# Performance work log

Hardware: AMD Instinct MI355X
Metric: run time of the kernel (lower is better)

Reference implementation:

```python
import jax, jax.numpy as jnp
import numpy as np

REG = 0.1  # config['reg']


def _poly_filter(s, gammas):
    # Horner evaluation of sum_k gammas[k] * s**k (monomial basis, depth K=len-1).
    out = jnp.full_like(s, gammas[-1])
    for k in range(gammas.shape[0] - 2, -1, -1):
        out = out * s + gammas[k]
    return out


def setup_inputs() -> dict:
    key = jax.random.key(0)
    k1, k2, k3, k4, k5 = jax.random.split(key, 5)
    B, H, N, R = 4, 8, 4096, 64
    U = jax.random.normal(k1, (B, H, N, R), dtype=jnp.float32)
    Sigma = jax.random.normal(k2, (B, H, 1, R), dtype=jnp.float32)
    svd_V = jax.random.normal(k3, (B, H, N, R), dtype=jnp.float32)
    V = jax.random.normal(k4, (B, H, N, R), dtype=jnp.float32)
    mask = jnp.ones((B, N), dtype=jnp.float32)
    # learnable polynomial coefficients; gamma_0 fixed to 1 (fixI=True)
    gammas = jnp.concatenate([jnp.ones((1,), jnp.float32),
                              0.1 * jax.random.normal(k5, (4,), dtype=jnp.float32)])
    return {"U": U, "Sigma": Sigma, "svd_V": svd_V, "V": V, "mask": mask, "gammas": gammas}


def reference(U, Sigma, svd_V, V, mask, gammas):
    # Q: softmax over rank dim r
    Q = jax.nn.softmax(U, axis=-1)                                      # [B,H,N,r]
    # K: masked softmax over sequence dim N
    Kmat = jax.nn.softmax(svd_V - 1e9 * (1.0 - mask[:, None, :, None]), axis=-2)
    S = jax.nn.sigmoid(Sigma)                                           # [B,H,1,r]
    graph_filter = _poly_filter(S, gammas)                              # [B,H,1,r]
    # linear-attention ordering: (Q*filt) @ (K^T @ V), never forms NxN
    KtV = jnp.einsum('bhnr,bhnd->bhrd', Kmat, V)                        # [B,H,r,d]
    X = jnp.einsum('bhnr,bhrd->bhnd', Q * graph_filter, KtV)            # [B,H,N,d]
    r = Q.shape[-1]
    eye = jnp.eye(r, dtype=Q.dtype)
    symQ = jnp.einsum('bhnr,bhns->bhrs', Q, Q) - eye
    ortho_loss = REG * jnp.mean(jnp.abs(symQ), axis=(1, 2, 3))
    symK = jnp.einsum('bhnr,bhns->bhrs', Kmat, Kmat) - eye
    ortho_loss = ortho_loss + REG * jnp.mean(jnp.abs(symK), axis=(1, 2, 3))
    return X, ortho_loss
```

## Files before the change

### kernel.cpp

```cpp
#include <hip/hip_runtime.h>
#include <math.h>

#define NB 4
#define NH 8
#define BHN 32
#define SN 4096
#define RR 64
#define REGC 0.1f

#define MCH 16
#define MROWS 256
#define XCH 32
#define XROWS 128

typedef short s16x8 __attribute__((ext_vector_type(8)));
typedef float f32x4 __attribute__((ext_vector_type(4)));

__device__ __forceinline__ float wave_sum(float v) {
    #pragma unroll
    for (int off = 32; off; off >>= 1) v += __shfl_xor(v, off, 64);
    return v;
}
__device__ __forceinline__ float wave_sum64(float v) {
    v += __int_as_float(__builtin_amdgcn_update_dpp(0, __float_as_int(v), 0x121, 0xf, 0xf, true));
    v += __int_as_float(__builtin_amdgcn_update_dpp(0, __float_as_int(v), 0x122, 0xf, 0xf, true));
    v += __int_as_float(__builtin_amdgcn_update_dpp(0, __float_as_int(v), 0x124, 0xf, 0xf, true));
    v += __int_as_float(__builtin_amdgcn_update_dpp(0, __float_as_int(v), 0x128, 0xf, 0xf, true));
    v += __shfl_xor(v, 16, 64);
    v += __shfl_xor(v, 32, 64);
    return v;
}
__device__ __forceinline__ float octet_sum(float v) {
    v += __int_as_float(__builtin_amdgcn_update_dpp(0, __float_as_int(v), 0xB1, 0xf, 0xf, true));
    v += __int_as_float(__builtin_amdgcn_update_dpp(0, __float_as_int(v), 0x4E, 0xf, 0xf, true));
    v += __shfl_xor(v, 4, 64);
    return v;
}
__device__ __forceinline__ float fastrcp(float x) {
    float r; asm("v_rcp_f32 %0, %1" : "=v"(r) : "v"(x)); return r;
}
__device__ __forceinline__ unsigned short f2bf(float x) {
    unsigned int u = __float_as_uint(x);
    u += 0x7FFFu + ((u >> 16) & 1u);
    return (unsigned short)(u >> 16);
}
__device__ __forceinline__ float bf2f(unsigned short h) {
    return __uint_as_float(((unsigned int)h) << 16);
}
__device__ __forceinline__ unsigned int pkbf(float lo, float hi) {
    unsigned int r;
    asm("v_cvt_pk_bf16_f32 %0, %1, %2" : "=v"(r) : "v"(lo), "v"(hi));
    return r;
}
__device__ __forceinline__ void barrier_nodrain() {
    asm volatile("s_waitcnt lgkmcnt(0)" ::: "memory");
    __builtin_amdgcn_s_barrier();
}
__device__ __forceinline__ s16x8 ldfrag(const unsigned int* p) {
    uint4 r = *(const uint4*)p;
    return __builtin_bit_cast(s16x8, r);
}
__device__ __forceinline__ int swz(int row, int blk) {
    return (row << 5) + (((blk ^ (row & 7))) << 2);
}
__device__ __forceinline__ uint4 pack8(const float* x) {
    return make_uint4(pkbf(x[0], x[1]), pkbf(x[2], x[3]),
                      pkbf(x[4], x[5]), pkbf(x[6], x[7]));
}

#define PH 0
#define VH 2048
#define QH 4096
__launch_bounds__(512, 4)
__global__ void k_main(const float* __restrict__ U, const float* __restrict__ sv,
                       const float* __restrict__ V, const float* __restrict__ mask,
                       float* __restrict__ ktv_part, float* __restrict__ symk_part,
                       float* __restrict__ symq_part, float* __restrict__ colsum_part) {
    __shared__ __align__(16) unsigned int sm[12288];
    const int chunk = blockIdx.x, bh = blockIdx.y, b = bh >> 3;
    const int t = threadIdx.x, l = t & 63, w = t >> 6;
    const int r15 = l & 15, quad = l >> 4;
    const int ni = w & 3, mi0 = (w >> 2) << 1;
    const size_t rowbase = (size_t)bh * SN * RR;
    const int row0 = chunk * MROWS;

    float csum = 0.0f;
    f32x4 aKV[2], aSK[2], aSQ[2];
    #pragma unroll
    for (int j = 0; j < 2; j++) {
        aKV[j] = (f32x4){0.f, 0.f, 0.f, 0.f};
        aSK[j] = (f32x4){0.f, 0.f, 0.f, 0.f};
        aSQ[j] = (f32x4){0.f, 0.f, 0.f, 0.f};
    }

    float bu[2][8], bx[2][8], bv[2][8], bm[2][8];
    #pragma unroll
    for (int i = 0; i < 8; i++) {
        const size_t off = rowbase + (size_t)(row0 + 8 * w + i) * RR + l;
        bu[0][i] = __builtin_nontemporal_load(&U[off]);
        bx[0][i] = __builtin_nontemporal_load(&sv[off]);
        bv[0][i] = __builtin_nontemporal_load(&V[off]);
        bm[0][i] = mask[b * SN + row0 + 8 * w + i];
    }

    #pragma unroll
    for (int s = 0; s < 4; s++) {
        const int cur = s & 1, nxt = cur ^ 1;
        const int nb = row0 + s * 64;
        const int bufb = cur * 6144;
        if (s < 3) {
            #pragma unroll
            for (int i = 0; i < 8; i++) {
                const size_t off = rowbase + (size_t)(nb + 64 + 8 * w + i) * RR + l;
                bu[nxt][i] = __builtin_nontemporal_load(&U[off]);
                bx[nxt][i] = __builtin_nontemporal_load(&sv[off]);
                bv[nxt][i] = __builtin_nontemporal_load(&V[off]);
                bm[nxt][i] = mask[b * SN + nb + 64 + 8 * w + i];
            }
        }
        float q[8], p[8];
        #pragma unroll
        for (int i = 0; i < 8; i++) {
            const float eu = __expf(bu[cur][i]);
            q[i] = eu * fastrcp(wave_sum64(eu));
        }
        #pragma unroll
        for (int i = 0; i < 8; i++) {
            p[i] = __expf(bx[cur][i] - 1e9f * (1.0f - bm[cur][i]));
            csum += p[i];
        }
        const uint4 ph = pack8(p);
        const uint4 vh = pack8(bv[cur]);
        const uint4 qh = pack8(q);
        const int wbase = bufb + (l << 5) + ((w ^ (l & 7)) << 2);
        *(uint4*)(sm + PH + wbase) = ph;
        *(uint4*)(sm + VH + wbase) = vh;
        *(uint4*)(sm + QH + wbase) = qh;
        barrier_nodrain();
        #pragma unroll
        for (int ks = 0; ks < 2; ks++) {
            const int ub = ks * 4 + quad;
            s16x8 Ah[2], AQ[2];
            #pragma unroll
            for (int j = 0; j < 2; j++) {
                const int oa = bufb + swz((mi0 + j) * 16 + r15, ub);
                Ah[j] = ldfrag(sm + PH + oa);
                AQ[j] = ldfrag(sm + QH + oa);
            }
            const int ob = bufb + swz(ni * 16 + r15, ub);
            const s16x8 Bvh = ldfrag(sm + VH + ob);
            const s16x8 Bph = ldfrag(sm + PH + ob);
            const s16x8 Bq  = ldfrag(sm + QH + ob);
            #pragma unroll
            for (int j = 0; j < 2; j++) {
                aKV[j] = __builtin_amdgcn_mfma_f32_16x16x32_bf16(Ah[j], Bvh, aKV[j], 0, 0, 0);
                aSK[j] = __builtin_amdgcn_mfma_f32_16x16x32_bf16(Ah[j], Bph, aSK[j], 0, 0, 0);
                aSQ[j] = __builtin_amdgcn_mfma_f32_16x16x32_bf16(AQ[j], Bq,  aSQ[j], 0, 0, 0);
            }
        }
    }
    const size_t pb = ((size_t)bh * MCH + chunk) * 4096;
    #pragma unroll
    for (int j = 0; j < 2; j++)
        #pragma unroll
        for (int r = 0; r < 4; r++) {
            const int e = ((mi0 + j) * 16 + quad * 4 + r) * 64 + ni * 16 + r15;
            ktv_part[pb + e]  = aKV[j][r];
            symk_part[pb + e] = aSK[j][r];
            symq_part[pb + e] = aSQ[j][r];
        }
    barrier_nodrain();
    float* smf = (float*)sm;
    smf[w * 64 + l] = csum;
    barrier_nodrain();
    if (w == 0) {
        float scol = 0.f;
        #pragma unroll
        for (int j = 0; j < 8; j++) scol += smf[j * 64 + l];
        colsum_part[(bh * MCH + chunk) * 64 + l] = scol;
    }
}

__global__ void k_finalize(const float* __restrict__ ktv_part, const float* __restrict__ symk_part,
                           const float* __restrict__ symq_part, const float* __restrict__ colsum_part,
                           const float* __restrict__ Sigma, const float* __restrict__ gammas,
                           unsigned short* __restrict__ ktvt_hi, unsigned short* __restrict__ ktvt_lo,
                           float* __restrict__ loss_part) {
    const int rb = blockIdx.x, bh = blockIdx.y, t = threadIdx.x;
    const int e = t & 127;
    const int h = t >> 7;
    const int idx = rb * 128 + e;
    float kv = 0.f, sk = 0.f, sq = 0.f;
    #pragma unroll
    for (int cc = 0; cc < 8; cc++) {
        const int ch = h * 8 + cc;
        const size_t pb = ((size_t)bh * MCH + ch) * 4096 + idx;
        kv += ktv_part[pb]; sk += symk_part[pb]; sq += symq_part[pb];
    }
    float csp = 0.f;
    if (t < 128) {
        const int col = t & 63, hc = t >> 6;
        #pragma unroll
        for (int cc = 0; cc < 8; cc++)
            csp += colsum_part[(bh * MCH + hc * 8 + cc) * 64 + col];
    }
    __shared__ float red[128][3];
    __shared__ float cs[64];
    __shared__ float smr[2];
    if (h == 1) { red[e][0] = kv; red[e][1] = sk; red[e][2] = sq; }
    if (t >= 64 && t < 128) cs[t - 64] = csp;
    __syncthreads();
    if (h == 0) { kv += red[e][0]; sk += red[e][1]; sq += red[e][2]; }
    if (t < 64) cs[t] += csp;
    __syncthreads();
    float lsum = 0.f;
    if (h == 0) {
        const int r = idx >> 6, c = idx & 63;
        const float iSr = fastrcp(cs[r]), iSc = fastrcp(cs[c]);
        const float g0 = gammas[0], g1 = gammas[1], g2 = gammas[2], g3 = gammas[3], g4 = gammas[4];
        const float sg = fastrcp(1.0f + __expf(-Sigma[bh * 64 + r]));
        float f = g4; f = f * sg + g3; f = f * sg + g2; f = f * sg + g1; f = f * sg + g0;
        const float kvf = kv * iSr * f;
        const unsigned short hi = f2bf(kvf);
        ktvt_hi[bh * 4096 + c * 64 + r] = hi;
        ktvt_lo[bh * 4096 + c * 64 + r] = f2bf(kvf - bf2f(hi));
        const float eye = (r == c) ? 1.0f : 0.0f;
        lsum = fabsf(sk * iSr * iSc - eye) + fabsf(sq - eye);
    }
    lsum = wave_sum(lsum);
    if ((t & 63) == 0 && t < 128) smr[t >> 6] = lsum;
    __syncthreads();
    if (t == 0) loss_part[bh * 32 + rb] = smr[0] + smr[1];
}

__launch_bounds__(512, 4)
__global__ void k_xq(const float* __restrict__ U,
                     const unsigned short* __restrict__ ktvt_hi,
                     const unsigned short* __restrict__ ktvt_lo,
                     const float* __restrict__ loss_part,
                     float* __restrict__ Xout, float* __restrict__ loss) {
    __shared__ __align__(16) unsigned int sm[4096];
    __shared__ float smr8[8];
    const int chunk = blockIdx.x, bh = blockIdx.y;
    const int t = threadIdx.x, l = t & 63, w = t >> 6;
    const int r15 = l & 15, quad = l >> 4;
    const int ni = w & 3, mi0 = (w >> 2) << 1;
    const size_t rowbase = (size_t)bh * SN * RR;
    const int row0 = chunk * XROWS;
    const int nl = 8 * w + (l >> 3);
    const int c0 = (l & 7) * 8;

    if (chunk == 0 && bh == 0) {
        float lv = loss_part[t * 2] + loss_part[t * 2 + 1];
        lv = wave_sum(lv);
        if ((t & 63) == 0) smr8[t >> 6] = lv;
    }

    s16x8 Bh[2], Bl[2];
    #pragma unroll
    for (int ks = 0; ks < 2; ks++) {
        const int idx = (ni * 16 + r15) * 64 + ks * 32 + quad * 8;
        Bh[ks] = __builtin_bit_cast(s16x8, *(const uint4*)(ktvt_hi + (size_t)bh * 4096 + idx));
        Bl[ks] = __builtin_bit_cast(s16x8, *(const uint4*)(ktvt_lo + (size_t)bh * 4096 + idx));
    }

    float4 ba[2], bb[2];
    {
        const float* src = U + rowbase + (size_t)(row0 + nl) * RR + c0;
        ba[0] = *(const float4*)src;
        bb[0] = *(const float4*)(src + 4);
    }

    #pragma unroll
    for (int s = 0; s < 2; s++) {
        const int cur = s & 1, nxt = cur ^ 1;
        const int nb = row0 + s * 64;
        const int bufb = cur * 2048;
        if (s < 1) {
            const float* src = U + rowbase + (size_t)(nb + 64 + nl) * RR + c0;
            ba[nxt] = *(const float4*)src;
            bb[nxt] = *(const float4*)(src + 4);
        }
        float e[8];
        e[0] = __expf(ba[cur].x); e[1] = __expf(ba[cur].y);
        e[2] = __expf(ba[cur].z); e[3] = __expf(ba[cur].w);
        e[4] = __expf(bb[cur].x); e[5] = __expf(bb[cur].y);
        e[6] = __expf(bb[cur].z); e[7] = __expf(bb[cur].w);
        float loc = 0.f;
        #pragma unroll
        for (int i = 0; i < 8; i++) loc += e[i];
        const float inv = fastrcp(octet_sum(loc));
        #pragma unroll
        for (int i = 0; i < 8; i++) e[i] *= inv;
        *(uint4*)(sm + bufb + swz(nl, l & 7)) = pack8(e);
        barrier_nodrain();
        if (s == 0 && chunk == 0 && bh == 0 && t < 4)
            loss[t] = (REGC / (NH * 64.0f * 64.0f)) * (smr8[2 * t] + smr8[2 * t + 1]);
        f32x4 acc[2];
        acc[0] = (f32x4){0.f, 0.f, 0.f, 0.f};
        acc[1] = (f32x4){0.f, 0.f, 0.f, 0.f};
        #pragma unroll
        for (int ks = 0; ks < 2; ks++) {
            #pragma unroll
            for (int jj = 0; jj < 2; jj++) {
                const int oa = bufb + swz((mi0 + jj) * 16 + r15, ks * 4 + quad);
                const s16x8 Ah = ldfrag(sm + oa);
                acc[jj] = __builtin_amdgcn_mfma_f32_16x16x32_bf16(Ah, Bh[ks], acc[jj], 0, 0, 0);
                acc[jj] = __builtin_amdgcn_mfma_f32_16x16x32_bf16(Ah, Bl[ks], acc[jj], 0, 0, 0);
            }
        }
        #pragma unroll
        for (int jj = 0; jj < 2; jj++)
            #pragma unroll
            for (int r = 0; r < 4; r++) {
                const int n = nb + (mi0 + jj) * 16 + quad * 4 + r;
                __builtin_nontemporal_store(acc[jj][r],
                    &Xout[rowbase + (size_t)n * RR + ni * 16 + r15]);
            }
    }
}

extern "C" void kernel_launch(void* const* d_in, const int* in_sizes, int n_in,
                              void* d_out, int out_size, void* d_ws, size_t ws_size,
                              hipStream_t stream) {
    (void)in_sizes; (void)n_in; (void)out_size; (void)ws_size;
    const float* U      = (const float*)d_in[0];
    const float* Sigma  = (const float*)d_in[1];
    const float* sv     = (const float*)d_in[2];
    const float* V      = (const float*)d_in[3];
    const float* mask   = (const float*)d_in[4];
    const float* gammas = (const float*)d_in[5];

    float* X    = (float*)d_out;
    float* loss = X + (size_t)BHN * SN * RR;

    float* ws          = (float*)d_ws;
    float* ktv_part    = ws;
    float* symk_part   = ktv_part + (size_t)BHN * MCH * 4096;
    float* symq_part   = symk_part + (size_t)BHN * MCH * 4096;
    float* colsum_part = symq_part + (size_t)BHN * MCH * 4096;
    float* loss_part   = colsum_part + BHN * MCH * 64;
    unsigned short* ktvt_hi = (unsigned short*)(loss_part + 1024);
    unsigned short* ktvt_lo = ktvt_hi + BHN * 4096;

    hipLaunchKernelGGL(k_main, dim3(MCH, BHN), dim3(512), 0, stream,
                       U, sv, V, mask, ktv_part, symk_part, symq_part, colsum_part);
    hipLaunchKernelGGL(k_finalize, dim3(32, BHN), dim3(256), 0, stream,
                       ktv_part, symk_part, symq_part, colsum_part, Sigma, gammas,
                       ktvt_hi, ktvt_lo, loss_part);
    hipLaunchKernelGGL(k_xq, dim3(XCH, BHN), dim3(512), 0, stream,
                       U, ktvt_hi, ktvt_lo, loss_part, X, loss);
}
```

Baseline: 158.7 us.

## Store bf16 softmax(U) from main kernel and reuse it in X kernel

The main kernel, which already computes the row softmax of U, now also writes Q as bf16 to a workspace buffer. The X kernel loads this bf16 Q directly into shared memory, with no reread of fp32 U and no repeated exp/normalize. This halves the bytes the X kernel reads but adds a 16 MB scattered 2-byte store stream to the main kernel. Total memory traffic is roughly unchanged.

```diff
diff --git a/kernel.cpp b/kernel.cpp
--- a/kernel.cpp
+++ b/kernel.cpp
@@ -30,12 +30,6 @@
     v += __shfl_xor(v, 32, 64);
     return v;
 }
-__device__ __forceinline__ float octet_sum(float v) {
-    v += __int_as_float(__builtin_amdgcn_update_dpp(0, __float_as_int(v), 0xB1, 0xf, 0xf, true));
-    v += __int_as_float(__builtin_amdgcn_update_dpp(0, __float_as_int(v), 0x4E, 0xf, 0xf, true));
-    v += __shfl_xor(v, 4, 64);
-    return v;
-}
 __device__ __forceinline__ float fastrcp(float x) {
     float r; asm("v_rcp_f32 %0, %1" : "=v"(r) : "v"(x)); return r;
 }
@@ -75,7 +69,8 @@
 __global__ void k_main(const float* __restrict__ U, const float* __restrict__ sv,
                        const float* __restrict__ V, const float* __restrict__ mask,
                        float* __restrict__ ktv_part, float* __restrict__ symk_part,
-                       float* __restrict__ symq_part, float* __restrict__ colsum_part) {
+                       float* __restrict__ symq_part, float* __restrict__ colsum_part,
+                       unsigned short* __restrict__ qg) {
     __shared__ __align__(16) unsigned int sm[12288];
     const int chunk = blockIdx.x, bh = blockIdx.y, b = bh >> 3;
     const int t = threadIdx.x, l = t & 63, w = t >> 6;
@@ -132,6 +127,15 @@
         const uint4 ph = pack8(p);
         const uint4 vh = pack8(bv[cur]);
         const uint4 qh = pack8(q);
+        {
+            unsigned short* qrow = qg + ((size_t)bh * SN + nb + 8 * w) * RR + l;
+            const unsigned int qw[4] = {qh.x, qh.y, qh.z, qh.w};
+            #pragma unroll
+            for (int i = 0; i < 4; i++) {
+                __builtin_nontemporal_store((unsigned short)(qw[i] & 0xffffu), qrow + (2 * i) * RR);
+                __builtin_nontemporal_store((unsigned short)(qw[i] >> 16),     qrow + (2 * i + 1) * RR);
+            }
+        }
         const int wbase = bufb + (l << 5) + ((w ^ (l & 7)) << 2);
         *(uint4*)(sm + PH + wbase) = ph;
         *(uint4*)(sm + VH + wbase) = vh;
@@ -234,7 +238,7 @@
 }
 
 __launch_bounds__(512, 4)
-__global__ void k_xq(const float* __restrict__ U,
+__global__ void k_xq(const unsigned short* __restrict__ qg,
                      const unsigned short* __restrict__ ktvt_hi,
                      const unsigned short* __restrict__ ktvt_lo,
                      const float* __restrict__ loss_part,
@@ -248,13 +252,11 @@
     const size_t rowbase = (size_t)bh * SN * RR;
     const int row0 = chunk * XROWS;
     const int nl = 8 * w + (l >> 3);
-    const int c0 = (l & 7) * 8;
-
-    if (chunk == 0 && bh == 0) {
-        float lv = loss_part[t * 2] + loss_part[t * 2 + 1];
-        lv = wave_sum(lv);
-        if ((t & 63) == 0) smr8[t >> 6] = lv;
-    }
+    const int c0h = l & 7;
+
+    const uint4* qg4 = (const uint4*)qg;
+    const uint4 q0 = qg4[((size_t)bh * SN + row0) * 8 + t];
+    const uint4 q1 = qg4[((size_t)bh * SN + row0 + 64) * 8 + t];
 
     s16x8 Bh[2], Bl[2];
     #pragma unroll
@@ -264,38 +266,23 @@
         Bl[ks] = __builtin_bit_cast(s16x8, *(const uint4*)(ktvt_lo + (size_t)bh * 4096 + idx));
     }
 
-    float4 ba[2], bb[2];
-    {
-        const float* src = U + rowbase + (size_t)(row0 + nl) * RR + c0;
-        ba[0] = *(const float4*)src;
-        bb[0] = *(const float4*)(src + 4);
-    }
+    float lv = 0.f;
+    if (chunk == 0 && bh == 0) {
+        lv = loss_part[t * 2] + loss_part[t * 2 + 1];
+        lv = wave_sum(lv);
+        if ((t & 63) == 0) smr8[t >> 6] = lv;
+    }
+
+    *(uint4*)(sm + swz(nl, c0h)) = q0;
+    *(uint4*)(sm + 2048 + swz(nl, c0h)) = q1;
+    __syncthreads();
+    if (chunk == 0 && bh == 0 && t < 4)
+        loss[t] = (REGC / (NH * 64.0f * 64.0f)) * (smr8[2 * t] + smr8[2 * t + 1]);
 
     #pragma unroll
     for (int s = 0; s < 2; s++) {
-        const int cur = s & 1, nxt = cur ^ 1;
         const int nb = row0 + s * 64;
-        const int bufb = cur * 2048;
-        if (s < 1) {
-            const float* src = U + rowbase + (size_t)(nb + 64 + nl) * RR + c0;
-            ba[nxt] = *(const float4*)src;
-            bb[nxt] = *(const float4*)(src + 4);
-        }
-        float e[8];
-        e[0] = __expf(ba[cur].x); e[1] = __expf(ba[cur].y);
-        e[2] = __expf(ba[cur].z); e[3] = __expf(ba[cur].w);
-        e[4] = __expf(bb[cur].x); e[5] = __expf(bb[cur].y);
-        e[6] = __expf(bb[cur].z); e[7] = __expf(bb[cur].w);
-        float loc = 0.f;
-        #pragma unroll
-        for (int i = 0; i < 8; i++) loc += e[i];
-        const float inv = fastrcp(octet_sum(loc));
-        #pragma unroll
-        for (int i = 0; i < 8; i++) e[i] *= inv;
-        *(uint4*)(sm + bufb + swz(nl, l & 7)) = pack8(e);
-        barrier_nodrain();
-        if (s == 0 && chunk == 0 && bh == 0 && t < 4)
-            loss[t] = (REGC / (NH * 64.0f * 64.0f)) * (smr8[2 * t] + smr8[2 * t + 1]);
+        const int bufb = s * 2048;
         f32x4 acc[2];
         acc[0] = (f32x4){0.f, 0.f, 0.f, 0.f};
         acc[1] = (f32x4){0.f, 0.f, 0.f, 0.f};
@@ -342,12 +329,13 @@
     float* loss_part   = colsum_part + BHN * MCH * 64;
     unsigned short* ktvt_hi = (unsigned short*)(loss_part + 1024);
     unsigned short* ktvt_lo = ktvt_hi + BHN * 4096;
+    unsigned short* qg      = ktvt_lo + BHN * 4096;
 
     hipLaunchKernelGGL(k_main, dim3(MCH, BHN), dim3(512), 0, stream,
-                       U, sv, V, mask, ktv_part, symk_part, symq_part, colsum_part);
+                       U, sv, V, mask, ktv_part, symk_part, symq_part, colsum_part, qg);
     hipLaunchKernelGGL(k_finalize, dim3(32, BHN), dim3(256), 0, stream,
                        ktv_part, symk_part, symq_part, colsum_part, Sigma, gammas,
                        ktvt_hi, ktvt_lo, loss_part);
     hipLaunchKernelGGL(k_xq, dim3(XCH, BHN), dim3(512), 0, stream,
-                       U, ktvt_hi, ktvt_lo, loss_part, X, loss);
-}
+                       qg, ktvt_hi, ktvt_lo, loss_part, X, loss);
+}
```

Result: no change. 160.8 us (+1.3%).
